# Performance work log

Hardware: AMD Instinct MI355X
Metric: run time of the kernel (lower is better)

The kernel has to match this reference:

```python
import jax, jax.numpy as jnp
import numpy as np

D_MODEL = 1024
NUM_HEADS = 16
OUT_SHAPE = (64,)            # ControlGate `shape`; d_head = prod(OUT_SHAPE)
BANK_SIZE = 16
TOP_K = 2
BATCH, SEQ = 8, 4096
D_OUT = NUM_HEADS * int(np.prod(OUT_SHAPE))  # 1024


def setup_inputs() -> dict:
    key = jax.random.key(0)
    k1, k2, k3, k4 = jax.random.split(key, 4)
    tensor = jax.random.normal(k1, (BATCH, SEQ, D_MODEL), dtype=jnp.float32)
    sel_idx = jax.random.randint(k2, (BATCH, TOP_K), 0, BANK_SIZE)
    sel_probs = jax.random.uniform(k3, (BATCH, TOP_K), dtype=jnp.float32)
    sel_probs = sel_probs / jnp.sum(sel_probs, axis=-1, keepdims=True)
    W = jax.random.normal(k4, (BANK_SIZE, D_MODEL, D_OUT), dtype=jnp.float32) * 0.02
    b = jnp.zeros((BANK_SIZE, D_OUT), dtype=jnp.float32)
    return {"tensor": tensor, "sel_idx": sel_idx, "sel_probs": sel_probs, "W": W, "b": b}


def reference(tensor, sel_idx, sel_probs, W, b):
    # --- VirtualMakeHeads: bank-selected (virtual) linear projection ---
    # Superimpose the selected weight banks per batch element.
    W_sel = W[sel_idx]                    # (B, K, d_model, d_out)  irregular gather
    b_sel = b[sel_idx]                    # (B, K, d_out)
    W_eff = jnp.einsum('bk,bkio->bio', sel_probs, W_sel)   # (B, d_model, d_out)
    b_eff = jnp.einsum('bk,bko->bo', sel_probs, b_sel)     # (B, d_out)
    logits = jnp.einsum('bsi,bio->bso', tensor, W_eff) + b_eff[:, None, :]
    # reshape to heads: (B, S, num_heads, d_head)
    logits = logits.reshape(*logits.shape[:-1], NUM_HEADS, -1)
    # --- ControlGate: unflatten last dim into OUT_SHAPE ---
    logits = logits.reshape(*logits.shape[:-1], *OUT_SHAPE)
    # DropoutLogits with p=0.0 (eval) is identity.
    # activation == 'sigmoid'
    return jax.nn.sigmoid(logits)
```

## Files before the change

### kernel.cpp

```cpp
#include <hip/hip_runtime.h>
#include <hip/hip_bf16.h>

#define B_  8
#define S_  4096
#define DM  1024
#define DO  1024

typedef __attribute__((ext_vector_type(4))) float f32x4;
typedef __attribute__((ext_vector_type(8))) short bf16x8;

__device__ inline unsigned int pkbf(float a, float b) {
    __hip_bfloat162 h = __float22bfloat162_rn(float2{a, b});
    union { __hip_bfloat162 h2; unsigned int u; } cv;
    cv.h2 = h;
    return cv.u;
}


__global__ __launch_bounds__(256) void prep_xpack(
    const float* __restrict__ X, unsigned short* __restrict__ xpack)
{
    const int bm = blockIdx.y, b = blockIdx.z;
    const int t = threadIdx.x;
    const int r  = t & 127;
    const int kt = blockIdx.x * 2 + (t >> 7);
    const float* src = X + ((size_t)(b * S_ + bm * 128 + r)) * DM + kt * 32;
    char* dst = (char*)xpack + ((size_t)((b * 32 + bm) * 32 + kt)) * 8192 + r * 64;
    const int q = (r >> 1) & 3;
    #pragma unroll
    for (int g = 0; g < 4; ++g) {
        float4 a = *reinterpret_cast<const float4*>(src + g * 8);
        float4 c = *reinterpret_cast<const float4*>(src + g * 8 + 4);
        uint4 u;
        u.x = pkbf(a.x, a.y); u.y = pkbf(a.z, a.w);
        u.z = pkbf(c.x, c.y); u.w = pkbf(c.z, c.w);
        *reinterpret_cast<uint4*>(dst + ((g ^ q) << 4)) = u;
    }
}

__global__ __launch_bounds__(256) void prep_wpack(
    const float* __restrict__ W, const int* __restrict__ sel_idx,
    const float* __restrict__ sel_probs, unsigned short* __restrict__ wpack)
{
    const int nb = blockIdx.y, b = blockIdx.z;
    const int i0 = sel_idx[b*2+0], i1 = sel_idx[b*2+1];
    const float p0 = sel_probs[b*2+0], p1 = sel_probs[b*2+1];
    const int t = threadIdx.x;
    const int c  = t & 127;
    const int kt = blockIdx.x * 2 + (t >> 7);
    const int o = nb * 128 + c;
    const float* w0 = W + (size_t)i0 * DM * DO + (size_t)(kt * 32) * DO + o;
    const float* w1 = W + (size_t)i1 * DM * DO + (size_t)(kt * 32) * DO + o;
    char* dst = (char*)wpack + ((size_t)((b * 8 + nb) * 32 + kt)) * 8192 + c * 64;
    const int q = (c >> 1) & 3;
    #pragma unroll
    for (int g = 0; g < 4; ++g) {
        float v[8];
        #pragma unroll
        for (int j = 0; j < 8; ++j)
            v[j] = p0 * w0[(size_t)(g * 8 + j) * DO] + p1 * w1[(size_t)(g * 8 + j) * DO];
        uint4 u;
        u.x = pkbf(v[0], v[1]); u.y = pkbf(v[2], v[3]);
        u.z = pkbf(v[4], v[5]); u.w = pkbf(v[6], v[7]);
        *reinterpret_cast<uint4*>(dst + ((g ^ q) << 4)) = u;
    }
}

__global__ __launch_bounds__(256) void prep_beff(
    const float* __restrict__ bias, const int* __restrict__ sel_idx,
    const float* __restrict__ sel_probs, float* __restrict__ beff)
{
    const int b = blockIdx.x;
    const int i0 = sel_idx[b*2+0], i1 = sel_idx[b*2+1];
    const float p0 = sel_probs[b*2+0], p1 = sel_probs[b*2+1];
    for (int o = threadIdx.x; o < DO; o += blockDim.x)
        beff[(size_t)b * DO + o] = p0 * bias[(size_t)i0 * DO + o]
                                 + p1 * bias[(size_t)i1 * DO + o];
}

__global__ __launch_bounds__(256, 4) void gemm128(
    const unsigned short* __restrict__ xpack, const unsigned short* __restrict__ wpack,
    const float* __restrict__ beff, float* __restrict__ out)
{
    __shared__ char lds[32768];

    const int id = blockIdx.x;
    const int swz = (id & 7) * 256 + (id >> 3);
    const int b  = swz >> 8;
    const int bm = (swz >> 3) & 31;
    const int nb = swz & 7;

    const int t = threadIdx.x;
    const int wave = t >> 6, lane = t & 63;
    const int wm = wave >> 1, wn = wave & 1;
    const int fr = lane & 15, fq = lane >> 4;

    const char* xt = (const char*)xpack + ((size_t)((b * 32 + bm) * 32)) * 8192;
    const char* wt = (const char*)wpack + ((size_t)((b * 8 + nb) * 32)) * 8192;

    const int q   = (fr >> 1) & 3;
    const int rdA = (wm * 64 + fr) * 64 + ((fq ^ q) << 4);
    const int rdB = (wn * 64 + fr) * 64 + ((fq ^ q) << 4);

    f32x4 acc[4][4] = {};

#define GLOAD(SRC, DST)                                                        \
    __builtin_amdgcn_global_load_lds(                                          \
        (const __attribute__((address_space(1))) void*)(SRC),                  \
        (__attribute__((address_space(3))) void*)(DST), 16, 0, 0)

#define STAGE(KT, OFF)                                                         \
    {   const char* ga = xt + (size_t)(KT) * 8192 + wave * 2048 + lane * 16;   \
        const char* gb = wt + (size_t)(KT) * 8192 + wave * 2048 + lane * 16;   \
        char* la = lds + (OFF) + wave * 2048;                                  \
        char* lb = lds + 16384 + (OFF) + wave * 2048;                          \
        GLOAD(ga, la); GLOAD(ga + 1024, la + 1024);                            \
        GLOAD(gb, lb); GLOAD(gb + 1024, lb + 1024); }

    STAGE(0, 0);
    __syncthreads();

    for (int kt = 0; kt < 32; ++kt) {
        const int cur = (kt & 1) * 8192;
        const int nxt = 8192 - cur;

        if (kt < 31) { STAGE(kt + 1, nxt); }

        bf16x8 bk[4];
        #pragma unroll
        for (int nf = 0; nf < 4; ++nf)
            bk[nf] = *reinterpret_cast<const bf16x8*>(lds + 16384 + cur + rdB + nf * 1024);
        #pragma unroll
        for (int m = 0; m < 4; ++m) {
            bf16x8 af = *reinterpret_cast<const bf16x8*>(lds + cur + rdA + m * 1024);
            #pragma unroll
            for (int nf = 0; nf < 4; ++nf)
                acc[m][nf] = __builtin_amdgcn_mfma_f32_16x16x32_bf16(af, bk[nf], acc[m][nf], 0, 0, 0);
        }

        __syncthreads();
    }

    const float* be = beff + (size_t)b * DO + nb * 128 + wn * 64;
    float bv[4];
    #pragma unroll
    for (int nf = 0; nf < 4; ++nf) bv[nf] = be[nf * 16 + fr];

    float* ob = out + ((size_t)(b * S_ + bm * 128 + wm * 64)) * DO + nb * 128 + wn * 64;
    #pragma unroll
    for (int m = 0; m < 4; ++m) {
        #pragma unroll
        for (int nf = 0; nf < 4; ++nf) {
            const int col = nf * 16 + fr;
            #pragma unroll
            for (int r = 0; r < 4; ++r) {
                const int row = m * 16 + fq * 4 + r;
                const float xv = acc[m][nf][r] + bv[nf];
                ob[(size_t)row * DO + col] = 1.0f / (1.0f + __expf(-xv));
            }
        }
    }
#undef GLOAD
#undef STAGE
}

__global__ __launch_bounds__(256) void prep_wpack_f(
    const float* __restrict__ W, const int* __restrict__ sel_idx,
    const float* __restrict__ sel_probs, unsigned short* __restrict__ wpack)
{
    const int kt = blockIdx.x, nb = blockIdx.y, b = blockIdx.z;
    const int i0 = sel_idx[b*2+0], i1 = sel_idx[b*2+1];
    const float p0 = sel_probs[b*2+0], p1 = sel_probs[b*2+1];
    const int t = threadIdx.x;
    const int col = t & 127;
    const int gh  = t >> 7;
    const int o = nb * 128 + col;
    const float* w0 = W + (size_t)i0 * DM * DO + (size_t)(kt * 32) * DO + o;
    const float* w1 = W + (size_t)i1 * DM * DO + (size_t)(kt * 32) * DO + o;
    char* tile = (char*)wpack + ((size_t)((b * 8 + nb) * 32 + kt)) * 8192;
    const int q = (col >> 1) & 3;
    #pragma unroll
    for (int gg = 0; gg < 2; ++gg) {
        const int g = gh * 2 + gg;
        float v[8];
        #pragma unroll
        for (int j = 0; j < 8; ++j)
            v[j] = p0 * w0[(size_t)(g * 8 + j) * DO] + p1 * w1[(size_t)(g * 8 + j) * DO];
        uint4 u;
        u.x = pkbf(v[0], v[1]); u.y = pkbf(v[2], v[3]);
        u.z = pkbf(v[4], v[5]); u.w = pkbf(v[6], v[7]);
        *reinterpret_cast<uint4*>(tile + col * 64 + ((g ^ q) << 4)) = u;
    }
}

__global__ __launch_bounds__(256, 4) void gemm4(
    const float* __restrict__ X, const unsigned short* __restrict__ wpack,
    const float* __restrict__ beff, float* __restrict__ out)
{
    __shared__ char lds[32768];
    const int id = blockIdx.x;
    const int swz = (id & 7) * 256 + (id >> 3);
    const int b  = swz >> 8;
    const int bm = (swz >> 3) & 31;
    const int nb = swz & 7;
    const int t = threadIdx.x;
    const int wave = t >> 6, lane = t & 63;
    const int wm = wave >> 1, wn = wave & 1;
    const int fr = lane & 15, fq = lane >> 4;
    const int s_row = t >> 1;
    const int s_h   = t & 1;
    const float* xrow = X + ((size_t)(b * S_ + bm * 128 + s_row)) * DM + s_h * 16;
    const int sq = (s_row >> 1) & 3;
    const int wrA0 = s_row * 64 + (((s_h * 2 + 0) ^ sq) << 4);
    const int wrA1 = s_row * 64 + (((s_h * 2 + 1) ^ sq) << 4);
    const char* wtile = (const char*)wpack + ((size_t)((b * 8 + nb) * 32)) * 8192;
    const int axor = (fr >> 1) & 3;
    const int rdA = (wm * 64 + fr) * 64 + ((fq ^ axor) << 4);
    const int rdB = (wn * 64 + fr) * 64 + ((fq ^ axor) << 4);
    f32x4 acc[4][4] = {};
    float4 ax0, ax1, ax2, ax3;
#define LOAD_X(KT)                                                            \
    {   const float* s = xrow + (KT) * 32;                                    \
        ax0 = *reinterpret_cast<const float4*>(s);                            \
        ax1 = *reinterpret_cast<const float4*>(s + 4);                        \
        ax2 = *reinterpret_cast<const float4*>(s + 8);                        \
        ax3 = *reinterpret_cast<const float4*>(s + 12); }
#define STAGE_B(KT, BOFF)                                                     \
    {   const char* gB = wtile + (size_t)(KT) * 8192;                         \
        _Pragma("unroll")                                                     \
        for (int r = 0; r < 2; ++r)                                           \
            __builtin_amdgcn_global_load_lds(                                 \
                (const __attribute__((address_space(1))) void*)(gB + (wave*2+r)*1024 + lane*16), \
                (__attribute__((address_space(3))) void*)(lds + (BOFF) + (wave*2+r)*1024),       \
                16, 0, 0); }
#define WRITE_A(AOFF)                                                         \
    {   uint4 u0, u1;                                                         \
        u0.x = pkbf(ax0.x, ax0.y); u0.y = pkbf(ax0.z, ax0.w);                 \
        u0.z = pkbf(ax1.x, ax1.y); u0.w = pkbf(ax1.z, ax1.w);                 \
        u1.x = pkbf(ax2.x, ax2.y); u1.y = pkbf(ax2.z, ax2.w);                 \
        u1.z = pkbf(ax3.x, ax3.y); u1.w = pkbf(ax3.z, ax3.w);                 \
        *reinterpret_cast<uint4*>(lds + (AOFF) + wrA0) = u0;                  \
        *reinterpret_cast<uint4*>(lds + (AOFF) + wrA1) = u1; }
    LOAD_X(0);
    __builtin_amdgcn_sched_barrier(0);
    STAGE_B(0, 16384);
    __builtin_amdgcn_sched_barrier(0);
    WRITE_A(0);
    __syncthreads();
    for (int kt = 0; kt < 32; ++kt) {
        const int cur = (kt & 1) * 8192;
        const int nxt = 8192 - cur;
        if (kt < 31) {
            LOAD_X(kt + 1);
            __builtin_amdgcn_sched_barrier(0);
            STAGE_B(kt + 1, 16384 + nxt);
            __builtin_amdgcn_sched_barrier(0);
        }
        bf16x8 bf[4];
        #pragma unroll
        for (int nf = 0; nf < 4; ++nf)
            bf[nf] = *reinterpret_cast<const bf16x8*>(lds + 16384 + cur + rdB + nf * 1024);
        #pragma unroll
        for (int m = 0; m < 4; ++m) {
            bf16x8 af = *reinterpret_cast<const bf16x8*>(lds + cur + rdA + m * 1024);
            #pragma unroll
            for (int nf = 0; nf < 4; ++nf)
                acc[m][nf] = __builtin_amdgcn_mfma_f32_16x16x32_bf16(af, bf[nf], acc[m][nf], 0, 0, 0);
        }
        if (kt < 31) { WRITE_A(nxt); }
        __syncthreads();
    }
    const float* be = beff + (size_t)b * DO + nb * 128 + wn * 64;
    float bv[4];
    #pragma unroll
    for (int nf = 0; nf < 4; ++nf) bv[nf] = be[nf * 16 + fr];
    float* ob = out + ((size_t)(b * S_ + bm * 128 + wm * 64)) * DO + nb * 128 + wn * 64;
    #pragma unroll
    for (int m = 0; m < 4; ++m) {
        #pragma unroll
        for (int nf = 0; nf < 4; ++nf) {
            const int col = nf * 16 + fr;
            #pragma unroll
            for (int r = 0; r < 4; ++r) {
                const int row = m * 16 + fq * 4 + r;
                const float xv = acc[m][nf][r] + bv[nf];
                ob[(size_t)row * DO + col] = 1.0f / (1.0f + __expf(-xv));
            }
        }
    }
#undef LOAD_X
#undef STAGE_B
#undef WRITE_A
}

extern "C" void kernel_launch(void* const* d_in, const int* in_sizes, int n_in,
                              void* d_out, int out_size, void* d_ws, size_t ws_size,
                              hipStream_t stream) {
    const float* tensor    = (const float*)d_in[0];
    const int*   sel_idx   = (const int*)d_in[1];
    const float* sel_probs = (const float*)d_in[2];
    const float* W         = (const float*)d_in[3];
    const float* bias      = (const float*)d_in[4];
    float* out = (float*)d_out;

    const size_t XP = (size_t)8192 * 8192;
    const size_t WP = (size_t)2048 * 8192;
    const size_t NEED = XP + WP + (size_t)B_ * DO * 4;

    if (ws_size >= NEED) {
        unsigned short* xpack = (unsigned short*)d_ws;
        unsigned short* wpack = (unsigned short*)((char*)d_ws + XP);
        float* beff = (float*)((char*)d_ws + XP + WP);

        hipLaunchKernelGGL(prep_xpack, dim3(16, 32, 8), dim3(256), 0, stream,
                           tensor, xpack);
        hipLaunchKernelGGL(prep_wpack, dim3(16, 8, 8), dim3(256), 0, stream,
                           W, sel_idx, sel_probs, wpack);
        hipLaunchKernelGGL(prep_beff, dim3(8), dim3(256), 0, stream,
                           bias, sel_idx, sel_probs, beff);
        hipLaunchKernelGGL(gemm128, dim3(2048), dim3(256), 0, stream,
                           xpack, wpack, beff, out);
    } else {
        unsigned short* wpack = (unsigned short*)d_ws;
        float* beff = (float*)((char*)d_ws + (size_t)8 * 8 * 32 * 8192);
        hipLaunchKernelGGL(prep_wpack_f, dim3(32, 8, 8), dim3(256), 0, stream,
                           W, sel_idx, sel_probs, wpack);
        hipLaunchKernelGGL(prep_beff, dim3(8), dim3(256), 0, stream,
                           bias, sel_idx, sel_probs, beff);
        hipLaunchKernelGGL(gemm4, dim3(2048), dim3(256), 0, stream,
                           tensor, wpack, beff, out);
    }
}
```

Before: 146.7 us.

## Triple-buffer LDS in GEMM with two-stage-ahead prefetch and partial vmcnt waits

Changes the GEMM main loop from double to triple buffering in LDS, so tiles are prefetched two k-steps ahead. The single __syncthreads is replaced by explicit waits and a raw barrier: s_waitcnt vmcnt(4) lets the most recent stage's loads stay in flight across the barrier. The aim is to hide global-to-LDS latency better. In exchange, LDS per block grows to 48KB and launch bounds drop from 4 to 3 blocks per CU, which lowers occupancy.

```diff
diff --git a/kernel.cpp b/kernel.cpp
--- a/kernel.cpp
+++ b/kernel.cpp
@@ -78,11 +78,11 @@
                                  + p1 * bias[(size_t)i1 * DO + o];
 }
 
-__global__ __launch_bounds__(256, 4) void gemm128(
+__global__ __launch_bounds__(256, 3) void gemm128r(
     const unsigned short* __restrict__ xpack, const unsigned short* __restrict__ wpack,
     const float* __restrict__ beff, float* __restrict__ out)
 {
-    __shared__ char lds[32768];
+    __shared__ char lds[49152];
 
     const int id = blockIdx.x;
     const int swz = (id & 7) * 256 + (id >> 3);
@@ -100,7 +100,7 @@
 
     const int q   = (fr >> 1) & 3;
     const int rdA = (wm * 64 + fr) * 64 + ((fq ^ q) << 4);
-    const int rdB = (wn * 64 + fr) * 64 + ((fq ^ q) << 4);
+    const int rdB = 24576 + (wn * 64 + fr) * 64 + ((fq ^ q) << 4);
 
     f32x4 acc[4][4] = {};
 
@@ -109,36 +109,45 @@
         (const __attribute__((address_space(1))) void*)(SRC),                  \
         (__attribute__((address_space(3))) void*)(DST), 16, 0, 0)
 
-#define STAGE(KT, OFF)                                                         \
+#define STAGE(KT, SLOT)                                                        \
     {   const char* ga = xt + (size_t)(KT) * 8192 + wave * 2048 + lane * 16;   \
         const char* gb = wt + (size_t)(KT) * 8192 + wave * 2048 + lane * 16;   \
-        char* la = lds + (OFF) + wave * 2048;                                  \
-        char* lb = lds + 16384 + (OFF) + wave * 2048;                          \
+        char* la = lds + (SLOT) + wave * 2048;                                 \
+        char* lb = lds + 24576 + (SLOT) + wave * 2048;                         \
         GLOAD(ga, la); GLOAD(ga + 1024, la + 1024);                            \
         GLOAD(gb, lb); GLOAD(gb + 1024, lb + 1024); }
 
     STAGE(0, 0);
-    __syncthreads();
-
+    STAGE(1, 8192);
+    asm volatile("s_waitcnt vmcnt(4)" ::: "memory");
+    __builtin_amdgcn_s_barrier();
+
+    int sR = 0, sN2 = 16384;
+
+    #pragma unroll 1
     for (int kt = 0; kt < 32; ++kt) {
-        const int cur = (kt & 1) * 8192;
-        const int nxt = 8192 - cur;
-
-        if (kt < 31) { STAGE(kt + 1, nxt); }
+        if (kt < 30) { STAGE(kt + 2, sN2); }
+        __builtin_amdgcn_sched_barrier(0);
 
         bf16x8 bk[4];
         #pragma unroll
         for (int nf = 0; nf < 4; ++nf)
-            bk[nf] = *reinterpret_cast<const bf16x8*>(lds + 16384 + cur + rdB + nf * 1024);
+            bk[nf] = *reinterpret_cast<const bf16x8*>(lds + sR + rdB + nf * 1024);
         #pragma unroll
         for (int m = 0; m < 4; ++m) {
-            bf16x8 af = *reinterpret_cast<const bf16x8*>(lds + cur + rdA + m * 1024);
+            bf16x8 af = *reinterpret_cast<const bf16x8*>(lds + sR + rdA + m * 1024);
             #pragma unroll
             for (int nf = 0; nf < 4; ++nf)
                 acc[m][nf] = __builtin_amdgcn_mfma_f32_16x16x32_bf16(af, bk[nf], acc[m][nf], 0, 0, 0);
         }
 
-        __syncthreads();
+        asm volatile("s_waitcnt lgkmcnt(0)" ::: "memory");
+        if (kt < 30) { asm volatile("s_waitcnt vmcnt(4)" ::: "memory"); }
+        else         { asm volatile("s_waitcnt vmcnt(0)" ::: "memory"); }
+        __builtin_amdgcn_s_barrier();
+
+        sR  = (sR  == 16384) ? 0 : sR  + 8192;
+        sN2 = (sN2 == 16384) ? 0 : sN2 + 8192;
     }
 
     const float* be = beff + (size_t)b * DO + nb * 128 + wn * 64;
@@ -318,7 +327,7 @@
                            W, sel_idx, sel_probs, wpack);
         hipLaunchKernelGGL(prep_beff, dim3(8), dim3(256), 0, stream,
                            bias, sel_idx, sel_probs, beff);
-        hipLaunchKernelGGL(gemm128, dim3(2048), dim3(256), 0, stream,
+        hipLaunchKernelGGL(gemm128r, dim3(2048), dim3(256), 0, stream,
                            xpack, wpack, beff, out);
     } else {
         unsigned short* wpack = (unsigned short*)d_ws;
```

Result: slower. 154.0 us (+5.0%).
